# Kernel tuning notes

Measured on AMD Instinct MI355X. Metric: run time of the kernel, lower is better.

The kernel has to match this reference:

```python
import jax, jax.numpy as jnp
import numpy as np
import math

NUM_HEADS = 8
EMB = 256

def setup_inputs() -> dict:
    key = jax.random.key(0)
    ks = jax.random.split(key, 9)
    B_, N, C = 1024, 64, EMB  # 16 images * 64 windows, 8x8 window, C=256
    nW = 64
    q = jax.random.normal(ks[0], (B_, N, C), dtype=jnp.float32)
    k = jax.random.normal(ks[1], (B_, N, C), dtype=jnp.float32)
    v = jax.random.normal(ks[2], (B_, N, C), dtype=jnp.float32)
    mask = jax.random.normal(ks[3], (nW, N, N), dtype=jnp.float32)
    # MLP params (Linear: y = x @ W^T + b; we store W already transposed for x @ W)
    hid = 4 * C
    s1 = 1.0 / math.sqrt(C)
    s2 = 1.0 / math.sqrt(hid)
    w1 = jax.random.uniform(ks[4], (C, hid), minval=-s1, maxval=s1, dtype=jnp.float32)
    b1 = jax.random.uniform(ks[5], (hid,), minval=-s1, maxval=s1, dtype=jnp.float32)
    w2 = jax.random.uniform(ks[6], (hid, C), minval=-s2, maxval=s2, dtype=jnp.float32)
    b2 = jax.random.uniform(ks[7], (C,), minval=-s2, maxval=s2, dtype=jnp.float32)
    return {"q": q, "k": k, "v": v, "mask": mask, "H": 64, "W": 64,
            "w1": w1, "b1": b1, "w2": w2, "b2": b2}

def reference(q, k, v, mask, H, W, w1, b1, w2, b2):
    B_, N, C = q.shape
    h = NUM_HEADS
    d = C // h
    # separate heads: (B_, h, N, d)
    qh = q.reshape(B_, N, h, d).transpose(0, 2, 1, 3)
    kh = k.reshape(B_, N, h, d).transpose(0, 2, 1, 3)
    vh = v.reshape(B_, N, h, d).transpose(0, 2, 1, 3)
    attn = jnp.einsum('bhnd,bhmd->bhnm', qh, kh)  # raw scores
    nW = mask.shape[0]
    # additive window mask BEFORE scaling (faithful to original order)
    attn = attn.reshape(B_ // nW, nW, h, N, N) + mask[None, :, None, :, :]
    attn = attn.reshape(B_, h, N, N) / math.sqrt(d)
    attn = jax.nn.softmax(attn, axis=-1)
    out = jnp.einsum('bhnm,bhmd->bhnd', attn, vh)
    out = out.transpose(0, 2, 1, 3).reshape(B_, N, C)  # recombine heads
    # linear Mlp (dropout is identity at p=0.0); torch nn.GELU is exact erf
    hmid = jax.nn.gelu(out @ w1 + b1, approximate=False)
    out = out + (hmid @ w2 + b2)
    return out
```

## Files before the change

kernel.cpp:

```cpp
#include <hip/hip_runtime.h>
#include <hip/hip_bf16.h>
#include <cstdint>
#include <cstddef>

typedef __attribute__((ext_vector_type(8))) short bf16x8;
typedef __attribute__((ext_vector_type(4))) float f32x4;

static __device__ __forceinline__ unsigned short f2bf(float f) {
    __hip_bfloat16 h = __float2bfloat16(f);
    return *reinterpret_cast<unsigned short*>(&h);
}

static __device__ __forceinline__ f32x4 mfma_bf16(bf16x8 a, bf16x8 b, f32x4 c) {
    return __builtin_amdgcn_mfma_f32_16x16x32_bf16(a, b, c, 0, 0, 0);
}

static __device__ __forceinline__ bf16x8 pack8(float4 a, float4 b) {
    bf16x8 f;
    f[0]=(short)f2bf(a.x); f[1]=(short)f2bf(a.y); f[2]=(short)f2bf(a.z); f[3]=(short)f2bf(a.w);
    f[4]=(short)f2bf(b.x); f[5]=(short)f2bf(b.y); f[6]=(short)f2bf(b.z); f[7]=(short)f2bf(b.w);
    return f;
}

static __device__ __forceinline__ float gelu_erf(float v) {
    float s = v * 0.70710678118654752f;
    float a = fabsf(s);
    float t = __builtin_amdgcn_rcpf(1.0f + 0.3275911f * a);
    float poly = ((((1.061405429f * t - 1.453152027f) * t + 1.421413741f) * t
                   - 0.284496736f) * t + 0.254829592f) * t;
    float e = 1.0f - poly * __expf(-a * a);
    float erfv = copysignf(e, s);
    return 0.5f * v * (1.0f + erfv);
}

static __device__ __forceinline__ void load_lds16(const unsigned short* g, unsigned short* l) {
    __builtin_amdgcn_global_load_lds(
        (const __attribute__((address_space(1))) unsigned int*)g,
        (__attribute__((address_space(3))) unsigned int*)l, 16, 0, 0);
}

__global__ __launch_bounds__(256) void attn_kernel(
    const float* __restrict__ q, const float* __restrict__ k,
    const float* __restrict__ v, const float* __restrict__ mask,
    float* __restrict__ xout)
{
    __shared__ unsigned short Qs[64][40];
    __shared__ unsigned short Ks[64][40];
    __shared__ unsigned short Vt[32][72];
    __shared__ unsigned short Ps[64][72];

    const int tid  = threadIdx.x;
    const int b    = blockIdx.x >> 3;
    const int h    = blockIdx.x & 7;
    const int lane = tid & 63;
    const int l15  = lane & 15;
    const int g    = lane >> 4;
    const int w    = tid >> 6;

    {
        int row = tid >> 2;
        int seg = tid & 3;
        size_t base = ((size_t)(b * 64 + row)) * 256 + h * 32 + seg * 8;

        float4 a0 = *(const float4*)(q + base);
        float4 a1 = *(const float4*)(q + base + 4);
        unsigned short* p = &Qs[row][seg * 8];
        p[0]=f2bf(a0.x); p[1]=f2bf(a0.y); p[2]=f2bf(a0.z); p[3]=f2bf(a0.w);
        p[4]=f2bf(a1.x); p[5]=f2bf(a1.y); p[6]=f2bf(a1.z); p[7]=f2bf(a1.w);

        a0 = *(const float4*)(k + base);
        a1 = *(const float4*)(k + base + 4);
        p = &Ks[row][seg * 8];
        p[0]=f2bf(a0.x); p[1]=f2bf(a0.y); p[2]=f2bf(a0.z); p[3]=f2bf(a0.w);
        p[4]=f2bf(a1.x); p[5]=f2bf(a1.y); p[6]=f2bf(a1.z); p[7]=f2bf(a1.w);

        a0 = *(const float4*)(v + base);
        a1 = *(const float4*)(v + base + 4);
        int c = seg * 8;
        Vt[c + 0][row] = f2bf(a0.x);
        Vt[c + 1][row] = f2bf(a0.y);
        Vt[c + 2][row] = f2bf(a0.z);
        Vt[c + 3][row] = f2bf(a0.w);
        Vt[c + 4][row] = f2bf(a1.x);
        Vt[c + 5][row] = f2bf(a1.y);
        Vt[c + 6][row] = f2bf(a1.z);
        Vt[c + 7][row] = f2bf(a1.w);
    }
    __syncthreads();

    f32x4 s[4];
    {
        bf16x8 aQ = *(const bf16x8*)&Qs[w * 16 + l15][g * 8];
        #pragma unroll
        for (int ct = 0; ct < 4; ++ct) {
            bf16x8 bK = *(const bf16x8*)&Ks[ct * 16 + l15][g * 8];
            f32x4 z = {0.f, 0.f, 0.f, 0.f};
            s[ct] = mfma_bf16(aQ, bK, z);
        }
    }

    const float* mbase = mask + (size_t)(b & 63) * 4096;
    const float INV = 0.17677669529663688f;
    float rsum[4];
    #pragma unroll
    for (int r = 0; r < 4; ++r) {
        int row = w * 16 + g * 4 + r;
        float pr[4];
        #pragma unroll
        for (int ct = 0; ct < 4; ++ct)
            pr[ct] = (s[ct][r] + mbase[row * 64 + ct * 16 + l15]) * INV;
        float m = fmaxf(fmaxf(pr[0], pr[1]), fmaxf(pr[2], pr[3]));
        #pragma unroll
        for (int off = 1; off < 16; off <<= 1)
            m = fmaxf(m, __shfl_xor(m, off));
        float sum = 0.f;
        #pragma unroll
        for (int ct = 0; ct < 4; ++ct) { pr[ct] = __expf(pr[ct] - m); sum += pr[ct]; }
        #pragma unroll
        for (int off = 1; off < 16; off <<= 1)
            sum += __shfl_xor(sum, off);
        rsum[r] = sum;
        #pragma unroll
        for (int ct = 0; ct < 4; ++ct)
            Ps[row][ct * 16 + l15] = f2bf(pr[ct]);
    }

    f32x4 o[2] = {};
    #pragma unroll
    for (int ks = 0; ks < 2; ++ks) {
        bf16x8 pa = *(const bf16x8*)&Ps[w * 16 + l15][ks * 32 + g * 8];
        #pragma unroll
        for (int n = 0; n < 2; ++n) {
            bf16x8 vb = *(const bf16x8*)&Vt[n * 16 + l15][ks * 32 + g * 8];
            o[n] = mfma_bf16(pa, vb, o[n]);
        }
    }

    #pragma unroll
    for (int n = 0; n < 2; ++n) {
        #pragma unroll
        for (int r = 0; r < 4; ++r) {
            int row = w * 16 + g * 4 + r;
            xout[((size_t)(b * 64 + row)) * 256 + h * 32 + n * 16 + l15] =
                o[n][r] / rsum[r];
        }
    }
}

__global__ __launch_bounds__(256) void prep_w1(const float* __restrict__ src,
                                               unsigned short* __restrict__ dst)
{
    __shared__ float tile[64][65];
    const int kt = blockIdx.x, nb = blockIdx.y;
    const int t = threadIdx.x;
    const int r0 = t >> 4, c4 = (t & 15) * 4;
    #pragma unroll
    for (int p = 0; p < 4; ++p) {
        int kk = r0 + p * 16;
        float4 d = *(const float4*)(src + (size_t)(kt * 64 + kk) * 1024 + nb * 64 + c4);
        tile[kk][c4+0]=d.x; tile[kk][c4+1]=d.y; tile[kk][c4+2]=d.z; tile[kk][c4+3]=d.w;
    }
    __syncthreads();
    #pragma unroll
    for (int i = 0; i < 2; ++i) {
        int f = t + 256 * i;
        int ksl = f >> 8;
        int ntg = (f >> 6) & 3;
        int gv  = (f >> 4) & 3;
        int l15v = f & 15;
        int n_local = ntg * 16 + l15v;
        int k_local = ksl * 32 + gv * 8;
        int c  = nb * 2 + (ntg >> 1);
        int nt = ntg & 1;
        int ks = kt * 2 + ksl;
        unsigned short tmp[8];
        #pragma unroll
        for (int e = 0; e < 8; ++e) tmp[e] = f2bf(tile[k_local + e][n_local]);
        size_t off = (size_t)c * 8192 + (size_t)((ks * 2 + nt) * 512)
                   + (gv * 16 + l15v) * 8;
        *(bf16x8*)(dst + off) = *(const bf16x8*)tmp;
    }
}

__global__ __launch_bounds__(256) void prep_w2(const float* __restrict__ src,
                                               unsigned short* __restrict__ dst)
{
    __shared__ float tile[64][65];
    const int ob = blockIdx.x, kb = blockIdx.y;
    const int t = threadIdx.x;
    const int r0 = t >> 4, c4 = (t & 15) * 4;
    #pragma unroll
    for (int p = 0; p < 4; ++p) {
        int kk = r0 + p * 16;
        float4 d = *(const float4*)(src + (size_t)(kb * 64 + kk) * 256 + ob * 64 + c4);
        tile[kk][c4+0]=d.x; tile[kk][c4+1]=d.y; tile[kk][c4+2]=d.z; tile[kk][c4+3]=d.w;
    }
    __syncthreads();
    #pragma unroll
    for (int i = 0; i < 2; ++i) {
        int f = t + 256 * i;
        int ksl = f >> 8;
        int tq  = (f >> 6) & 3;
        int gv  = (f >> 4) & 3;
        int l15v = f & 15;
        int c_local = tq * 16 + l15v;
        int k_local = ksl * 32 + gv * 8;
        int c = kb * 2 + ksl;
        unsigned short tmp[8];
        #pragma unroll
        for (int e = 0; e < 8; ++e) tmp[e] = f2bf(tile[k_local + e][c_local]);
        size_t off = (size_t)c * 8192 + (size_t)((ob * 4 + tq) * 512)
                   + (gv * 16 + l15v) * 8;
        *(bf16x8*)(dst + off) = *(const bf16x8*)tmp;
    }
}

__global__ __launch_bounds__(512, 4) void mlp_fused(
    const float* __restrict__ xin, float* __restrict__ xio,
    const unsigned short* __restrict__ wt1, const float* __restrict__ b1,
    const unsigned short* __restrict__ wt2, const float* __restrict__ b2)
{
    __shared__ unsigned short w1c[2][8192];
    __shared__ unsigned short w2c[2][8192];
    __shared__ unsigned short Hs[128][40];

    const int tid  = threadIdx.x;
    const int lane = tid & 63;
    const int l15  = lane & 15;
    const int g    = lane >> 4;
    const int wid  = tid >> 6;
    const int wmo  = wid >> 2, wno = wid & 3;
    const int fb   = (g * 16 + l15) * 8;

    const size_t rowbase = (size_t)blockIdx.x * 128;

    auto stage = [&](const unsigned short* gbase, unsigned short* lbase) {
        #pragma unroll
        for (int i = 0; i < 2; ++i) {
            load_lds16(gbase + (i * 512 + tid) * 8,
                       lbase + (i * 512 + wid * 64) * 8);
        }
    };

    stage(wt1, &w1c[0][0]);
    stage(wt2, &w2c[0][0]);

    bf16x8 xf[8];
    {
        const float* xr = xin + (rowbase + wid * 16 + l15) * 256;
        #pragma unroll
        for (int ks = 0; ks < 8; ++ks) {
            float4 a0 = *(const float4*)(xr + ks * 32 + g * 8);
            float4 a1 = *(const float4*)(xr + ks * 32 + g * 8 + 4);
            xf[ks] = pack8(a0, a1);
        }
    }

    f32x4 oacc[4][4] = {};

    for (int hc = 0; hc < 32; ++hc) {
        const int cur = hc & 1;
        __syncthreads();

        if (hc < 31) {
            stage(wt1 + (size_t)(hc + 1) * 8192, &w1c[cur ^ 1][0]);
            stage(wt2 + (size_t)(hc + 1) * 8192, &w2c[cur ^ 1][0]);
        }

        f32x4 hacc[2] = {};
        #pragma unroll
        for (int ks = 0; ks < 8; ++ks) {
            bf16x8 b0  = *(const bf16x8*)&w1c[cur][(ks * 2 + 0) * 512 + fb];
            bf16x8 b1f = *(const bf16x8*)&w1c[cur][(ks * 2 + 1) * 512 + fb];
            hacc[0] = mfma_bf16(xf[ks], b0,  hacc[0]);
            hacc[1] = mfma_bf16(xf[ks], b1f, hacc[1]);
        }

        bf16x8 bF[4];
        #pragma unroll
        for (int t = 0; t < 4; ++t)
            bF[t] = *(const bf16x8*)&w2c[cur][(wno * 4 + t) * 512 + fb];

        #pragma unroll
        for (int nt = 0; nt < 2; ++nt) {
            int coll = nt * 16 + l15;
            float bias = b1[hc * 32 + coll];
            #pragma unroll
            for (int r = 0; r < 4; ++r) {
                float vv = gelu_erf(hacc[nt][r] + bias);
                Hs[wid * 16 + g * 4 + r][coll] = f2bf(vv);
            }
        }
        __syncthreads();

        bf16x8 aF[4];
        #pragma unroll
        for (int t = 0; t < 4; ++t)
            aF[t] = *(const bf16x8*)&Hs[wmo * 64 + t * 16 + l15][g * 8];
        #pragma unroll
        for (int mt = 0; mt < 4; ++mt)
            #pragma unroll
            for (int nt = 0; nt < 4; ++nt)
                oacc[mt][nt] = mfma_bf16(aF[mt], bF[nt], oacc[mt][nt]);
    }

    #pragma unroll
    for (int nt = 0; nt < 4; ++nt) {
        int col = wno * 64 + nt * 16 + l15;
        float bias = b2[col];
        #pragma unroll
        for (int mt = 0; mt < 4; ++mt) {
            #pragma unroll
            for (int r = 0; r < 4; ++r) {
                size_t idx = (rowbase + wmo * 64 + mt * 16 + g * 4 + r) * 256 + col;
                xio[idx] = oacc[mt][nt][r] + bias + xio[idx];
            }
        }
    }
}

extern "C" void kernel_launch(void* const* d_in, const int* in_sizes, int n_in,
                              void* d_out, int out_size, void* d_ws, size_t ws_size,
                              hipStream_t stream)
{
    const float* q    = (const float*)d_in[0];
    const float* k    = (const float*)d_in[1];
    const float* v    = (const float*)d_in[2];
    const float* mask = (const float*)d_in[3];
    const float* w1   = (const float*)d_in[6];
    const float* b1   = (const float*)d_in[7];
    const float* w2   = (const float*)d_in[8];
    const float* b2   = (const float*)d_in[9];

    float* xio = (float*)d_out;

    unsigned short* wt1 = (unsigned short*)d_ws;
    unsigned short* wt2 = wt1 + (size_t)1024 * 256;

    prep_w1<<<dim3(4, 16), 256, 0, stream>>>(w1, wt1);
    prep_w2<<<dim3(4, 16), 256, 0, stream>>>(w2, wt2);

    attn_kernel<<<8192, 256, 0, stream>>>(q, k, v, mask, xio);

    mlp_fused<<<512, 512, 0, stream>>>(xio, xio, wt1, b1, wt2, b2);
}
```

Measured before the change: 184.6 us.

## Make each wave own its 16 rows end to end, dropping a block barrier

The second GEMM is repartitioned so each wave computes the full 256-wide output for the same 16 rows it produced in the first GEMM. The hidden tile then stays wave-private in LDS, and the mid-iteration __syncthreads is removed. The b1 bias is also staged into shared memory once. In exchange, each wave now reads all 16 W2 fragments from LDS per chunk instead of 4, so LDS read traffic goes up, and there is no A-fragment reuse across N tiles.

```diff
diff --git a/kernel.cpp b/kernel.cpp
--- a/kernel.cpp
+++ b/kernel.cpp
@@ -222,14 +222,14 @@
 {
     __shared__ unsigned short w1c[2][8192];
     __shared__ unsigned short w2c[2][8192];
-    __shared__ unsigned short Hs[128][40];
+    __shared__ unsigned short Hs[8][16][36];
+    __shared__ float b1s[1024];
 
     const int tid  = threadIdx.x;
     const int lane = tid & 63;
     const int l15  = lane & 15;
     const int g    = lane >> 4;
     const int wid  = tid >> 6;
-    const int wmo  = wid >> 2, wno = wid & 3;
     const int fb   = (g * 16 + l15) * 8;
 
     const size_t rowbase = (size_t)blockIdx.x * 128;
@@ -244,6 +244,9 @@
 
     stage(wt1, &w1c[0][0]);
     stage(wt2, &w2c[0][0]);
+
+    b1s[tid]       = b1[tid];
+    b1s[tid + 512] = b1[tid + 512];
 
     bf16x8 xf[8];
     {
@@ -256,7 +259,7 @@
         }
     }
 
-    f32x4 oacc[4][4] = {};
+    f32x4 oacc[16] = {};
 
     for (int hc = 0; hc < 32; ++hc) {
         const int cur = hc & 1;
@@ -276,45 +279,33 @@
             hacc[1] = mfma_bf16(xf[ks], b1f, hacc[1]);
         }
 
-        bf16x8 bF[4];
-        #pragma unroll
-        for (int t = 0; t < 4; ++t)
-            bF[t] = *(const bf16x8*)&w2c[cur][(wno * 4 + t) * 512 + fb];
-
         #pragma unroll
         for (int nt = 0; nt < 2; ++nt) {
             int coll = nt * 16 + l15;
-            float bias = b1[hc * 32 + coll];
+            float bias = b1s[hc * 32 + coll];
             #pragma unroll
             for (int r = 0; r < 4; ++r) {
                 float vv = gelu_erf(hacc[nt][r] + bias);
-                Hs[wid * 16 + g * 4 + r][coll] = f2bf(vv);
+                Hs[wid][g * 4 + r][coll] = f2bf(vv);
             }
         }
-        __syncthreads();
-
-        bf16x8 aF[4];
-        #pragma unroll
-        for (int t = 0; t < 4; ++t)
-            aF[t] = *(const bf16x8*)&Hs[wmo * 64 + t * 16 + l15][g * 8];
-        #pragma unroll
-        for (int mt = 0; mt < 4; ++mt)
-            #pragma unroll
-            for (int nt = 0; nt < 4; ++nt)
-                oacc[mt][nt] = mfma_bf16(aF[mt], bF[nt], oacc[mt][nt]);
-    }
-
-    #pragma unroll
-    for (int nt = 0; nt < 4; ++nt) {
-        int col = wno * 64 + nt * 16 + l15;
+
+        bf16x8 aH = *(const bf16x8*)&Hs[wid][l15][g * 8];
+        #pragma unroll
+        for (int n = 0; n < 16; ++n) {
+            bf16x8 bF = *(const bf16x8*)&w2c[cur][n * 512 + fb];
+            oacc[n] = mfma_bf16(aH, bF, oacc[n]);
+        }
+    }
+
+    #pragma unroll
+    for (int n = 0; n < 16; ++n) {
+        int col = n * 16 + l15;
         float bias = b2[col];
         #pragma unroll
-        for (int mt = 0; mt < 4; ++mt) {
-            #pragma unroll
-            for (int r = 0; r < 4; ++r) {
-                size_t idx = (rowbase + wmo * 64 + mt * 16 + g * 4 + r) * 256 + col;
-                xio[idx] = oacc[mt][nt][r] + bias + xio[idx];
-            }
+        for (int r = 0; r < 4; ++r) {
+            size_t idx = (rowbase + wid * 16 + g * 4 + r) * 256 + col;
+            xio[idx] = oacc[n][r] + bias + xio[idx];
         }
     }
 }
```

New measurement: 170.0 us. 7.9% less time.
